# Kernel optimization log

Hardware: AMD Instinct MI355X
Metric: run time of the kernel (lower is better)

## Reference

```python
import jax, jax.numpy as jnp
import numpy as np

B, C, V, L = 32, 32, 207, 128
C_OUT = 32
ORDER = 2


def setup_inputs() -> dict:
    key = jax.random.key(0)
    ks = jax.random.split(key, 6)
    x = jax.random.normal(ks[0], (B, C, V, L), dtype=jnp.float32)
    A0 = jax.random.uniform(ks[1], (V, V), dtype=jnp.float32) / V
    A1 = jax.random.uniform(ks[2], (V, V), dtype=jnp.float32) / V
    A2 = jax.random.uniform(ks[3], (V, V), dtype=jnp.float32) / V
    c_in_total = (ORDER * 3 + 1) * C  # 224
    W = jax.random.normal(ks[4], (C_OUT, c_in_total), dtype=jnp.float32) * 0.05
    b = jax.random.normal(ks[5], (C_OUT,), dtype=jnp.float32) * 0.05
    return {"x": x, "A0": A0, "A1": A1, "A2": A2, "W": W, "b": b}


def _nconv(x, A):
    # x: [n, c, v, l], A: [v, w] -> [n, c, w, l]
    return jnp.einsum('ncvl,vw->ncwl', x, A)


def reference(x, A0, A1, A2, W, b):
    outs = [x]
    for A in (A0, A1, A2):
        x1 = _nconv(x, A)
        outs.append(x1)
        for _ in range(2, ORDER + 1):
            x1 = _nconv(x1, A)
            outs.append(x1)
    h = jnp.concatenate(outs, axis=1)  # [n, 7*C, v, l]
    # 1x1 Conv2d == channel-mixing matmul; dropout is identity in eval mode
    return jnp.einsum('ncvl,oc->novl', h, W) + b[None, :, None, None]
```

## Files before the change

kernel.cpp:

```cpp
#include <hip/hip_runtime.h>

#define VDIM 207
#define LDIM 128
#define VP 224
#define VL (VDIM*LDIM)
#define NC 1024
#define NPOINT (32*VL)
#define APITCH 232
#define SWZ(row, colb) ((row) * 464 + ((colb) ^ (((row) & 1) << 5)))

typedef unsigned short u16;
typedef unsigned int u32;
typedef __attribute__((ext_vector_type(4))) float f32x4;
typedef __attribute__((ext_vector_type(8))) short s16x8;

__device__ __forceinline__ u16 f2bf(float f) {
  u32 u = __float_as_uint(f);
  return (u16)((u + 0x7FFFu + ((u >> 16) & 1u)) >> 16);
}
__device__ __forceinline__ float bf2f(u16 h) {
  return __uint_as_float(((u32)h) << 16);
}

__global__ void k_prep(const float* __restrict__ A0, const float* __restrict__ A1,
                       const float* __restrict__ A2, const float* __restrict__ W,
                       u16* __restrict__ MT, float* __restrict__ WT,
                       u16* __restrict__ Wb) {
  int idx = blockIdx.x * 256 + threadIdx.x;
  if (idx < 3 * VP * VP) {
    int i = idx / (VP * VP);
    int r = idx % (VP * VP);
    int w = r / VP, v = r % VP;
    const float* A = (i == 0) ? A0 : ((i == 1) ? A1 : A2);
    float f = (w < VDIM && v < VDIM) ? A[v * VDIM + w] : 0.f;
    MT[(size_t)(2 * i) * (VP * VP) + r] = f2bf(f);
  } else {
    int j = idx - 3 * VP * VP;
    if (j < VP * 32) {
      int k = j >> 5, o = j & 31;
      WT[j] = W[o * 224 + k];
    } else if (j < 2 * VP * 32) {
      int j2 = j - VP * 32;
      Wb[j2] = f2bf(W[j2]);
    }
  }
}

__global__ void k_sq(const float* __restrict__ A0, const float* __restrict__ A1,
                     const float* __restrict__ A2, u16* __restrict__ MT) {
  int idx = blockIdx.x * 256 + threadIdx.x;
  if (idx >= 3 * VP * VP) return;
  int i = idx / (VP * VP), r = idx % (VP * VP);
  int w = r / VP, v = r % VP;
  const float* A = (i == 0) ? A0 : ((i == 1) ? A1 : A2);
  float s = 0.f;
  if (w < VDIM && v < VDIM) {
#pragma unroll 4
    for (int u = 0; u < VDIM; ++u) s += A[v * VDIM + u] * A[u * VDIM + w];
  }
  MT[(size_t)(2 * i + 1) * (VP * VP) + r] = f2bf(s);
}

__global__ __launch_bounds__(256) void k_xt(const float* __restrict__ x,
                                            u16* __restrict__ xT) {
  __shared__ float tile[64 * 130];
  int nc = blockIdx.x;
  const float* xs = x + (size_t)nc * VL;
  u16* xd = xT + (size_t)nc * (128 * VP);
  int tid = threadIdx.x;
  for (int ch = 0; ch < 4; ++ch) {
    int v0 = ch * 64;
    __syncthreads();
#pragma unroll
    for (int j = 0; j < 8; ++j) {
      int idx = j * 256 + tid;
      int vr = idx >> 5, c4 = idx & 31;
      int v = v0 + vr;
      float4 val = make_float4(0.f, 0.f, 0.f, 0.f);
      if (v < VDIM) val = *(const float4*)(xs + (size_t)v * LDIM + c4 * 4);
      float* trow = &tile[vr * 130 + c4 * 4];
      *(float2*)(trow) = make_float2(val.x, val.y);
      *(float2*)(trow + 2) = make_float2(val.z, val.w);
    }
    __syncthreads();
    int l = tid >> 1, h = tid & 1;
    int vbase = v0 + h * 32;
    if (vbase < VP) {
      u32 wd[16];
#pragma unroll
      for (int j = 0; j < 16; ++j) {
        int v = vbase + 2 * j;
        float f0 = (v < VDIM) ? tile[(h * 32 + 2 * j) * 130 + l] : 0.f;
        float f1 = (v + 1 < VDIM) ? tile[(h * 32 + 2 * j + 1) * 130 + l] : 0.f;
        wd[j] = (u32)f2bf(f0) | ((u32)f2bf(f1) << 16);
      }
      uint4* dst = (uint4*)(xd + (size_t)l * VP + vbase);
#pragma unroll
      for (int t = 0; t < 4; ++t)
        dst[t] = make_uint4(wd[4 * t], wd[4 * t + 1], wd[4 * t + 2], wd[4 * t + 3]);
    }
  }
}

__global__ __launch_bounds__(256, 4) void k_gemm2(const u16* __restrict__ xT,
                                                  const u16* __restrict__ MT,
                                                  u16* __restrict__ zbuf,
                                                  int j0, int jcount) {
  __shared__ __align__(16) u16 A_s[64 * APITCH];
  int tid = threadIdx.x;
  int lane = tid & 63, wn = tid >> 6;
  int lane15 = lane & 15, lgrp = lane >> 4;
  int nc = blockIdx.x;
  const u16* xg = xT + (size_t)nc * (128 * VP);
  int col0 = wn * 32 + lane15, col1 = col0 + 16;

  s16x8 bx0[7], bx1[7];
#pragma unroll
  for (int ks = 0; ks < 7; ++ks) {
    bx0[ks] = *(const s16x8*)(xg + (size_t)col0 * VP + ks * 32 + lgrp * 8);
    bx1[ks] = *(const s16x8*)(xg + (size_t)col1 * VP + ks * 32 + lgrp * 8);
  }

  const int niter = jcount * 4;
  for (int u = 0; u < niter; ++u) {
    int j = u >> 2, ch = u & 3;
    int rowbase = ch * 64;
    int nrows = (ch < 3) ? 64 : 16;
    const u16* Mg = MT + (size_t)(j0 + j) * (VP * VP) + (size_t)rowbase * VP;
    for (int t = tid; t < nrows * 28; t += 256) {
      int r = t / 28, cq = t - r * 28;
      *(uint4*)((char*)A_s + SWZ(r, cq * 16)) = *(const uint4*)(Mg + r * VP + cq * 8);
    }
    __syncthreads();

    int nmt = (ch < 3) ? 4 : 1;
    f32x4 acc[4][2];
#pragma unroll
    for (int m = 0; m < 4; ++m) {
      acc[m][0] = (f32x4){0.f, 0.f, 0.f, 0.f};
      acc[m][1] = (f32x4){0.f, 0.f, 0.f, 0.f};
    }
    for (int ks = 0; ks < 7; ++ks) {
      int colb = ks * 64 + lgrp * 16;
#pragma unroll
      for (int mt = 0; mt < 4; ++mt) {
        if (mt < nmt) {
          s16x8 af = *(const s16x8*)((char*)A_s + SWZ(mt * 16 + lane15, colb));
          asm("v_mfma_f32_16x16x32_bf16 %0, %1, %2, %0"
              : "+v"(acc[mt][0]) : "v"(af), "v"(bx0[ks]));
          asm("v_mfma_f32_16x16x32_bf16 %0, %1, %2, %0"
              : "+v"(acc[mt][1]) : "v"(af), "v"(bx1[ks]));
        }
      }
    }
    __syncthreads();

    u16* zg = zbuf + (size_t)j * ((size_t)NC * VL) + (size_t)nc * VL;
#pragma unroll
    for (int mt = 0; mt < 4; ++mt) {
      if (mt < nmt) {
#pragma unroll
        for (int nt = 0; nt < 2; ++nt) {
          f32x4 a = acc[mt][nt];
          int col = wn * 32 + nt * 16 + lane15;
          int wb = rowbase + mt * 16 + lgrp * 4;
          u16 u0 = f2bf(a.x), u1 = f2bf(a.y), u2 = f2bf(a.z), u3 = f2bf(a.w);
          if (wb + 0 < VDIM) zg[(wb + 0) * LDIM + col] = u0;
          if (wb + 1 < VDIM) zg[(wb + 1) * LDIM + col] = u1;
          if (wb + 2 < VDIM) zg[(wb + 2) * LDIM + col] = u2;
          if (wb + 3 < VDIM) zg[(wb + 3) * LDIM + col] = u3;
        }
      }
    }
  }
}

__global__ __launch_bounds__(512, 4) void k_mixm(const float* __restrict__ x,
                                                 const u16* __restrict__ zb,
                                                 const u16* __restrict__ Wb,
                                                 const float* __restrict__ bias,
                                                 float* __restrict__ out) {
  __shared__ __align__(16) u16 hT_s[128 * APITCH];
  __shared__ __align__(16) u16 tile[2][32 * 136];
  int tid = threadIdx.x;
  int bid = blockIdx.x;
  int n = bid / 207, pt = bid - n * 207;
  int p0 = pt * 128;
  int lane = tid & 63, wn = tid >> 6;
  int lane15 = lane & 15, lgrp = lane >> 4;

  s16x8 wa0[7], wa1[7];
#pragma unroll
  for (int ks = 0; ks < 7; ++ks) {
    wa0[ks] = *(const s16x8*)(Wb + lane15 * 224 + ks * 32 + lgrp * 8);
    wa1[ks] = *(const s16x8*)(Wb + (16 + lane15) * 224 + ks * 32 + lgrp * 8);
  }

#pragma unroll
  for (int t = 0; t < 2; ++t) {
    int j = t * 512 + tid;
    int c = j >> 5, q = j & 31;
    float4 v = *(const float4*)(x + (size_t)(n * 32 + c) * VL + p0 + q * 4);
    int sc = 2 * ((c >> 3) & 3);
    u16* tp = tile[0] + c * 136;
    *(u32*)(tp + ((q * 4) ^ sc)) = (u32)f2bf(v.x) | ((u32)f2bf(v.y) << 16);
    *(u32*)(tp + ((q * 4 + 2) ^ sc)) = (u32)f2bf(v.z) | ((u32)f2bf(v.w) << 16);
  }
  int zc = tid >> 4, zq = tid & 15;
  uint4 zvA = *(const uint4*)(zb + ((size_t)(n * 32) + zc) * VL + p0 + zq * 8);
  __syncthreads();

  int cur = 0;
  for (int g7 = 0; g7 < 7; ++g7) {
    uint4 zvB = zvA;
    if (g7 < 5)
      zvB = *(const uint4*)(zb + ((size_t)((g7 + 1) << 10) + n * 32 + zc) * VL + p0 + zq * 8);
#pragma unroll
    for (int t = 0; t < 4; ++t) {
      int j = t * 512 + tid;
      int cp = j & 15, p = j >> 4;
      int sc = 2 * ((cp >> 2) & 3);
      const u16* tp = tile[cur];
      u32 w = (u32)tp[(2 * cp) * 136 + (p ^ sc)] |
              ((u32)tp[(2 * cp + 1) * 136 + (p ^ sc)] << 16);
      *(u32*)(hT_s + p * APITCH + g7 * 32 + 2 * cp) = w;
    }
    if (g7 < 6) {
      int sc = 2 * ((zc >> 3) & 3);
      u16* tp = tile[cur ^ 1] + zc * 136;
      u32 zd[4] = {zvA.x, zvA.y, zvA.z, zvA.w};
#pragma unroll
      for (int t = 0; t < 4; ++t)
        *(u32*)(tp + ((zq * 8 + 2 * t) ^ sc)) = zd[t];
    }
    __syncthreads();
    zvA = zvB;
    cur ^= 1;
  }

  f32x4 acc[2];
  acc[0] = (f32x4){0.f, 0.f, 0.f, 0.f};
  acc[1] = (f32x4){0.f, 0.f, 0.f, 0.f};
  int colp = wn * 16 + lane15;
#pragma unroll
  for (int ks = 0; ks < 7; ++ks) {
    s16x8 bfrag = *(const s16x8*)(hT_s + colp * APITCH + ks * 32 + lgrp * 8);
    asm("v_mfma_f32_16x16x32_bf16 %0, %1, %2, %0"
        : "+v"(acc[0]) : "v"(wa0[ks]), "v"(bfrag));
    asm("v_mfma_f32_16x16x32_bf16 %0, %1, %2, %0"
        : "+v"(acc[1]) : "v"(wa1[ks]), "v"(bfrag));
  }

#pragma unroll
  for (int mt = 0; mt < 2; ++mt) {
#pragma unroll
    for (int j = 0; j < 4; ++j) {
      int o = mt * 16 + lgrp * 4 + j;
      out[(size_t)(n * 32 + o) * VL + p0 + colp] = acc[mt][j] + bias[o];
    }
  }
}

template <int MODE, int NZ>
__global__ __launch_bounds__(256, 4) void k_mix(const float* __restrict__ x,
                                                const u16* __restrict__ zb,
                                                const float* __restrict__ WT,
                                                const float* __restrict__ bias,
                                                float* __restrict__ out, int wk0) {
  int t = blockIdx.x * 256 + threadIdx.x;
  int pp = t * 2;
  int n = pp / VL;
  int rem = pp - n * VL;
  float* op = out + (size_t)n * 32 * VL + rem;
  f32x4 a0[8], a1[8];

  if (MODE == 0) {
#pragma unroll
    for (int j = 0; j < 8; ++j) {
      f32x4 bv = *(const f32x4*)(bias + 4 * j);
      a0[j] = bv;
      a1[j] = bv;
    }
    const float* xp = x + (size_t)n * 32 * VL + rem;
#pragma unroll
    for (int c0 = 0; c0 < 32; c0 += 4) {
      float2 v[4];
#pragma unroll
      for (int q = 0; q < 4; ++q)
        v[q] = *(const float2*)(xp + (size_t)(c0 + q) * VL);
#pragma unroll
      for (int q = 0; q < 4; ++q) {
        const float* wv = WT + (c0 + q) * 32;
#pragma unroll
        for (int j = 0; j < 8; ++j) {
          f32x4 w4 = *(const f32x4*)(wv + 4 * j);
          a0[j] += w4 * v[q].x;
          a1[j] += w4 * v[q].y;
        }
      }
    }
  } else {
#pragma unroll
    for (int j = 0; j < 8; ++j) {
#pragma unroll
      for (int q = 0; q < 4; ++q) {
        float2 r = *(const float2*)(op + (size_t)(4 * j + q) * VL);
        a0[j][q] = r.x;
        a1[j][q] = r.y;
      }
    }
  }

#pragma unroll 1
  for (int g = 0; g < NZ; ++g) {
    const u16* zp = zb + ((size_t)g * NC + (size_t)n * 32) * VL + rem;
    const float* wg = WT + (wk0 + g * 32) * 32;
#pragma unroll
    for (int c0 = 0; c0 < 32; c0 += 4) {
      u32 zv[4];
#pragma unroll
      for (int q = 0; q < 4; ++q)
        zv[q] = *(const u32*)(zp + (size_t)(c0 + q) * VL);
#pragma unroll
      for (int q = 0; q < 4; ++q) {
        float f0 = bf2f((u16)(zv[q] & 0xFFFFu));
        float f1 = bf2f((u16)(zv[q] >> 16));
        const float* wv = wg + (c0 + q) * 32;
#pragma unroll
        for (int j = 0; j < 8; ++j) {
          f32x4 w4 = *(const f32x4*)(wv + 4 * j);
          a0[j] += w4 * f0;
          a1[j] += w4 * f1;
        }
      }
    }
  }

#pragma unroll
  for (int j = 0; j < 8; ++j) {
#pragma unroll
    for (int q = 0; q < 4; ++q) {
      float2 r;
      r.x = a0[j][q];
      r.y = a1[j][q];
      *(float2*)(op + (size_t)(4 * j + q) * VL) = r;
    }
  }
}

extern "C" void kernel_launch(void* const* d_in, const int* in_sizes, int n_in,
                              void* d_out, int out_size, void* d_ws, size_t ws_size,
                              hipStream_t stream) {
  const float* x = (const float*)d_in[0];
  const float* A0 = (const float*)d_in[1];
  const float* A1 = (const float*)d_in[2];
  const float* A2 = (const float*)d_in[3];
  const float* W = (const float*)d_in[4];
  const float* b = (const float*)d_in[5];
  float* out = (float*)d_out;

  const size_t xT_sz = (size_t)NC * 128 * VP * 2;
  const size_t MT_sz = (size_t)6 * VP * VP * 2;
  const size_t WT_sz = (size_t)VP * 32 * 4;
  const size_t Wb_sz = (size_t)VP * 32 * 2;
  const size_t slot_sz = (size_t)NC * VL * 2;

  char* wp = (char*)d_ws;
  u16* xT = (u16*)wp; wp += (xT_sz + 255) & ~(size_t)255;
  u16* MT = (u16*)wp; wp += (MT_sz + 255) & ~(size_t)255;
  float* WT = (float*)wp; wp += (WT_sz + 255) & ~(size_t)255;
  u16* Wb = (u16*)wp; wp += (Wb_sz + 255) & ~(size_t)255;
  u16* zbuf = (u16*)wp;
  size_t base = (size_t)(wp - (char*)d_ws);
  bool bigws = ws_size >= base + 6 * slot_sz;

  k_prep<<<644, 256, 0, stream>>>(A0, A1, A2, W, MT, WT, Wb);
  k_sq<<<588, 256, 0, stream>>>(A0, A1, A2, MT);
  k_xt<<<NC, 256, 0, stream>>>(x, xT);
  if (bigws) {
    k_gemm2<<<NC, 256, 0, stream>>>(xT, MT, zbuf, 0, 6);
    k_mixm<<<32 * 207, 512, 0, stream>>>(x, zbuf, Wb, b, out);
  } else {
    const int mixgrid = NPOINT / 512;
    k_mix<0, 0><<<mixgrid, 256, 0, stream>>>(x, nullptr, WT, b, out, 32);
    for (int i = 0; i < 3; ++i) {
      k_gemm2<<<NC, 256, 0, stream>>>(xT, MT, zbuf, 2 * i, 2);
      k_mix<1, 2><<<mixgrid, 256, 0, stream>>>(nullptr, zbuf, WT, nullptr, out,
                                               (1 + 2 * i) * 32);
    }
  }
}
```

Baseline: 383.6 us.

## Coalesce k_sq, split k_xt across blocks, batch gemm preloads, drop z prefetch

k_sq now maps one block per (matrix, row v) and one thread per column w. Reads of A[u*V+w] are coalesced across threads, and the output index is rewritten to match. k_xt is split into four blocks per (n,c), one per 64-row chunk, to raise parallelism and remove the in-kernel chunk loop and its syncs. k_gemm2 issues its B-fragment loads with inline asm and a single waitcnt so they stay in flight together; k_mixm drops its one-step z-prefetch in favour of a load inside each iteration, which may expose more latency, and gains an unused n0 offset parameter.

```diff
diff --git a/kernel.cpp b/kernel.cpp
--- a/kernel.cpp
+++ b/kernel.cpp
@@ -46,59 +46,59 @@
   }
 }
 
-__global__ void k_sq(const float* __restrict__ A0, const float* __restrict__ A1,
-                     const float* __restrict__ A2, u16* __restrict__ MT) {
-  int idx = blockIdx.x * 256 + threadIdx.x;
-  if (idx >= 3 * VP * VP) return;
-  int i = idx / (VP * VP), r = idx % (VP * VP);
-  int w = r / VP, v = r % VP;
+__global__ __launch_bounds__(256) void k_sq(const float* __restrict__ A0,
+                                            const float* __restrict__ A1,
+                                            const float* __restrict__ A2,
+                                            u16* __restrict__ MT) {
+  int bid = blockIdx.x;
+  int i = bid / VP, v = bid - i * VP;
+  int w = threadIdx.x;
+  if (w >= VP) return;
   const float* A = (i == 0) ? A0 : ((i == 1) ? A1 : A2);
   float s = 0.f;
-  if (w < VDIM && v < VDIM) {
+  if (v < VDIM && w < VDIM) {
 #pragma unroll 4
     for (int u = 0; u < VDIM; ++u) s += A[v * VDIM + u] * A[u * VDIM + w];
   }
-  MT[(size_t)(2 * i + 1) * (VP * VP) + r] = f2bf(s);
+  MT[(size_t)(2 * i + 1) * (VP * VP) + w * VP + v] = f2bf(s);
 }
 
 __global__ __launch_bounds__(256) void k_xt(const float* __restrict__ x,
                                             u16* __restrict__ xT) {
   __shared__ float tile[64 * 130];
-  int nc = blockIdx.x;
+  int bid = blockIdx.x;
+  int nc = bid >> 2, ch = bid & 3;
   const float* xs = x + (size_t)nc * VL;
   u16* xd = xT + (size_t)nc * (128 * VP);
   int tid = threadIdx.x;
-  for (int ch = 0; ch < 4; ++ch) {
-    int v0 = ch * 64;
-    __syncthreads();
-#pragma unroll
-    for (int j = 0; j < 8; ++j) {
-      int idx = j * 256 + tid;
-      int vr = idx >> 5, c4 = idx & 31;
-      int v = v0 + vr;
-      float4 val = make_float4(0.f, 0.f, 0.f, 0.f);
-      if (v < VDIM) val = *(const float4*)(xs + (size_t)v * LDIM + c4 * 4);
-      float* trow = &tile[vr * 130 + c4 * 4];
-      *(float2*)(trow) = make_float2(val.x, val.y);
-      *(float2*)(trow + 2) = make_float2(val.z, val.w);
-    }
-    __syncthreads();
-    int l = tid >> 1, h = tid & 1;
-    int vbase = v0 + h * 32;
-    if (vbase < VP) {
-      u32 wd[16];
-#pragma unroll
-      for (int j = 0; j < 16; ++j) {
-        int v = vbase + 2 * j;
-        float f0 = (v < VDIM) ? tile[(h * 32 + 2 * j) * 130 + l] : 0.f;
-        float f1 = (v + 1 < VDIM) ? tile[(h * 32 + 2 * j + 1) * 130 + l] : 0.f;
-        wd[j] = (u32)f2bf(f0) | ((u32)f2bf(f1) << 16);
-      }
-      uint4* dst = (uint4*)(xd + (size_t)l * VP + vbase);
-#pragma unroll
-      for (int t = 0; t < 4; ++t)
-        dst[t] = make_uint4(wd[4 * t], wd[4 * t + 1], wd[4 * t + 2], wd[4 * t + 3]);
-    }
+  int v0 = ch * 64;
+#pragma unroll
+  for (int j = 0; j < 8; ++j) {
+    int idx = j * 256 + tid;
+    int vr = idx >> 5, c4 = idx & 31;
+    int v = v0 + vr;
+    float4 val = make_float4(0.f, 0.f, 0.f, 0.f);
+    if (v < VDIM) val = *(const float4*)(xs + (size_t)v * LDIM + c4 * 4);
+    float* trow = &tile[vr * 130 + c4 * 4];
+    *(float2*)(trow) = make_float2(val.x, val.y);
+    *(float2*)(trow + 2) = make_float2(val.z, val.w);
+  }
+  __syncthreads();
+  int l = tid >> 1, h = tid & 1;
+  int vbase = v0 + h * 32;
+  if (vbase < VP) {
+    u32 wd[16];
+#pragma unroll
+    for (int j = 0; j < 16; ++j) {
+      int v = vbase + 2 * j;
+      float f0 = (v < VDIM) ? tile[(h * 32 + 2 * j) * 130 + l] : 0.f;
+      float f1 = (v + 1 < VDIM) ? tile[(h * 32 + 2 * j + 1) * 130 + l] : 0.f;
+      wd[j] = (u32)f2bf(f0) | ((u32)f2bf(f1) << 16);
+    }
+    uint4* dst = (uint4*)(xd + (size_t)l * VP + vbase);
+#pragma unroll
+    for (int t = 0; t < 4; ++t)
+      dst[t] = make_uint4(wd[4 * t], wd[4 * t + 1], wd[4 * t + 2], wd[4 * t + 3]);
   }
 }
 
@@ -117,9 +117,16 @@
   s16x8 bx0[7], bx1[7];
 #pragma unroll
   for (int ks = 0; ks < 7; ++ks) {
-    bx0[ks] = *(const s16x8*)(xg + (size_t)col0 * VP + ks * 32 + lgrp * 8);
-    bx1[ks] = *(const s16x8*)(xg + (size_t)col1 * VP + ks * 32 + lgrp * 8);
-  }
+    const u16* p0 = xg + (size_t)col0 * VP + ks * 32 + lgrp * 8;
+    const u16* p1 = xg + (size_t)col1 * VP + ks * 32 + lgrp * 8;
+    asm volatile("global_load_dwordx4 %0, %1, off" : "=v"(bx0[ks]) : "v"(p0));
+    asm volatile("global_load_dwordx4 %0, %1, off" : "=v"(bx1[ks]) : "v"(p1));
+  }
+  asm volatile("s_waitcnt vmcnt(0)"
+               : "+v"(bx0[0]), "+v"(bx0[1]), "+v"(bx0[2]), "+v"(bx0[3]),
+                 "+v"(bx0[4]), "+v"(bx0[5]), "+v"(bx0[6]),
+                 "+v"(bx1[0]), "+v"(bx1[1]), "+v"(bx1[2]), "+v"(bx1[3]),
+                 "+v"(bx1[4]), "+v"(bx1[5]), "+v"(bx1[6]));
 
   const int niter = jcount * 4;
   for (int u = 0; u < niter; ++u) {
@@ -179,12 +186,13 @@
                                                  const u16* __restrict__ zb,
                                                  const u16* __restrict__ Wb,
                                                  const float* __restrict__ bias,
-                                                 float* __restrict__ out) {
+                                                 float* __restrict__ out, int n0) {
   __shared__ __align__(16) u16 hT_s[128 * APITCH];
   __shared__ __align__(16) u16 tile[2][32 * 136];
   int tid = threadIdx.x;
   int bid = blockIdx.x;
-  int n = bid / 207, pt = bid - n * 207;
+  int q7 = bid / 207, pt = bid - q7 * 207;
+  int n = n0 + q7;
   int p0 = pt * 128;
   int lane = tid & 63, wn = tid >> 6;
   int lane15 = lane & 15, lgrp = lane >> 4;
@@ -206,15 +214,14 @@
     *(u32*)(tp + ((q * 4) ^ sc)) = (u32)f2bf(v.x) | ((u32)f2bf(v.y) << 16);
     *(u32*)(tp + ((q * 4 + 2) ^ sc)) = (u32)f2bf(v.z) | ((u32)f2bf(v.w) << 16);
   }
+  __syncthreads();
+
+  int cur = 0;
   int zc = tid >> 4, zq = tid & 15;
-  uint4 zvA = *(const uint4*)(zb + ((size_t)(n * 32) + zc) * VL + p0 + zq * 8);
-  __syncthreads();
-
-  int cur = 0;
   for (int g7 = 0; g7 < 7; ++g7) {
-    uint4 zvB = zvA;
-    if (g7 < 5)
-      zvB = *(const uint4*)(zb + ((size_t)((g7 + 1) << 10) + n * 32 + zc) * VL + p0 + zq * 8);
+    uint4 zv;
+    if (g7 < 6)
+      zv = *(const uint4*)(zb + ((size_t)(g7 << 10) + n * 32 + zc) * VL + p0 + zq * 8);
 #pragma unroll
     for (int t = 0; t < 4; ++t) {
       int j = t * 512 + tid;
@@ -228,13 +235,12 @@
     if (g7 < 6) {
       int sc = 2 * ((zc >> 3) & 3);
       u16* tp = tile[cur ^ 1] + zc * 136;
-      u32 zd[4] = {zvA.x, zvA.y, zvA.z, zvA.w};
+      u32 zd[4] = {zv.x, zv.y, zv.z, zv.w};
 #pragma unroll
       for (int t = 0; t < 4; ++t)
         *(u32*)(tp + ((zq * 8 + 2 * t) ^ sc)) = zd[t];
     }
     __syncthreads();
-    zvA = zvB;
     cur ^= 1;
   }
 
@@ -375,11 +381,11 @@
   bool bigws = ws_size >= base + 6 * slot_sz;
 
   k_prep<<<644, 256, 0, stream>>>(A0, A1, A2, W, MT, WT, Wb);
-  k_sq<<<588, 256, 0, stream>>>(A0, A1, A2, MT);
-  k_xt<<<NC, 256, 0, stream>>>(x, xT);
+  k_sq<<<3 * VP, 256, 0, stream>>>(A0, A1, A2, MT);
+  k_xt<<<4 * NC, 256, 0, stream>>>(x, xT);
   if (bigws) {
     k_gemm2<<<NC, 256, 0, stream>>>(xT, MT, zbuf, 0, 6);
-    k_mixm<<<32 * 207, 512, 0, stream>>>(x, zbuf, Wb, b, out);
+    k_mixm<<<32 * 207, 512, 0, stream>>>(x, zbuf, Wb, b, out, 0);
   } else {
     const int mixgrid = NPOINT / 512;
     k_mix<0, 0><<<mixgrid, 256, 0, stream>>>(x, nullptr, WT, b, out, 32);
```

New measurement: 340.8 us. -11.2%, faster.
